# Performance work log

Hardware: AMD Instinct MI355X
Metric: run time of the kernel (lower is better)

Reference implementation:

```python
import jax, jax.numpy as jnp
import numpy as np

NUM_CHANNELS = 64
EMBED_DIM = 64
NUM_HEADS = 8


def _hilbert_filter(T):
    # scipy.signal.hilbert frequency-domain multiplier
    h = np.zeros(T, dtype=np.float32)
    if T % 2 == 0:
        h[0] = 1.0
        h[T // 2] = 1.0
        h[1:T // 2] = 2.0
    else:
        h[0] = 1.0
        h[1:(T + 1) // 2] = 2.0
    return jnp.asarray(h)


def setup_inputs() -> dict:
    key = jax.random.key(0)
    ks = jax.random.split(key, 12)
    B, C, T, E = 32, NUM_CHANNELS, 8192, EMBED_DIM
    inp = {
        "x": jax.random.normal(ks[0], (B, C, T), dtype=jnp.float32),
        "electrode_embeddings": jax.random.normal(ks[1], (C, E), dtype=jnp.float32),
        "w1": jax.random.normal(ks[2], (E, 2 * E), dtype=jnp.float32),
        "b1": jnp.zeros((2 * E,), dtype=jnp.float32),
        "w2": jax.random.normal(ks[3], (2 * E, E), dtype=jnp.float32),
        "b2": jnp.zeros((E,), dtype=jnp.float32),
        "in_proj_w": jax.random.normal(ks[4], (3 * E, E), dtype=jnp.float32) * (1.0 / np.sqrt(E)),
        "in_proj_b": jnp.zeros((3 * E,), dtype=jnp.float32),
        "out_proj_w": jax.random.normal(ks[5], (E, E), dtype=jnp.float32) * (1.0 / np.sqrt(E)),
        "out_proj_b": jnp.zeros((E,), dtype=jnp.float32),
    }
    return inp


def _connectivity(x):
    # x: (B, C, T) real. PLV_{ij} = |mean_t exp(i (phi_i - phi_j))|
    B, C, T = x.shape
    h = _hilbert_filter(T)
    analytic = jnp.fft.ifft(jnp.fft.fft(x, axis=-1) * h, axis=-1)  # complex64
    Z = analytic / jnp.abs(analytic)  # unit-magnitude phasors exp(i*phi)
    plv = jnp.abs(jnp.einsum("bit,bjt->bij", Z, jnp.conj(Z))) / T
    # original never fills the diagonal -> zero it
    eye = jnp.eye(C, dtype=plv.dtype)
    return plv * (1.0 - eye)


def _mha(h, in_proj_w, in_proj_b, out_proj_w, out_proj_b):
    # torch nn.MultiheadAttention, batch_first, self-attention
    B, N, E = h.shape
    H, D = NUM_HEADS, E // NUM_HEADS
    qkv = h @ in_proj_w.T + in_proj_b  # (B, N, 3E)
    q, k, v = jnp.split(qkv, 3, axis=-1)

    def heads(t):
        return t.reshape(B, N, H, D).transpose(0, 2, 1, 3)  # (B, H, N, D)

    q, k, v = heads(q), heads(k), heads(v)
    scores = jnp.einsum("bhqd,bhkd->bhqk", q, k) / jnp.sqrt(jnp.asarray(D, h.dtype))
    attn = jax.nn.softmax(scores, axis=-1)
    out = jnp.einsum("bhqk,bhkd->bhqd", attn, v)
    out = out.transpose(0, 2, 1, 3).reshape(B, N, E)
    return out @ out_proj_w.T + out_proj_b


def reference(x, electrode_embeddings, w1, b1, w2, b2,
              in_proj_w, in_proj_b, out_proj_w, out_proj_b):
    B = x.shape[0]
    connectivity = _connectivity(x)  # (B, C, C)
    node_features = jnp.broadcast_to(electrode_embeddings[None], (B,) + electrode_embeddings.shape)
    # GCN layer 1
    h1 = jnp.einsum("bij,bjf->bif", connectivity, node_features @ w1) + b1
    h1 = jax.nn.relu(h1)
    # GCN layer 2
    h2 = jnp.einsum("bij,bjf->bif", connectivity, h1 @ w2) + b2
    graph_features = _mha(h2, in_proj_w, in_proj_b, out_proj_w, out_proj_b)
    return connectivity, graph_features, h2
```

## Files before the change

kernel.cpp:

```cpp
#include <hip/hip_runtime.h>
#include <math.h>

#define T_LEN 8192
#define NS_G 8

typedef float  f32x4 __attribute__((ext_vector_type(4)));
typedef _Float16 f16x8 __attribute__((ext_vector_type(8)));
typedef float  cpx   __attribute__((ext_vector_type(2)));
typedef _Float16 f16h2 __attribute__((ext_vector_type(2)));

#define CADD(d, a, b) \
    asm("v_pk_add_f32 %0, %1, %2" : "=v"(d) : "v"(a), "v"(b))
#define CSUB(d, a, b) \
    asm("v_pk_add_f32 %0, %1, %2 neg_lo:[0,1] neg_hi:[0,1]" : "=v"(d) : "v"(a), "v"(b))
#define CFMA(d, s, a, b) \
    asm("v_pk_fma_f32 %0, %1, %2, %3" : "=v"(d) : "v"(s), "v"(a), "v"(b))
#define CMUL(d, x, w) do { cpx _t_;                                            \
    asm("v_pk_mul_f32 %0, %1, %2 op_sel:[0,0] op_sel_hi:[1,0]"                 \
        : "=v"(_t_) : "v"(x), "v"(w));                                         \
    asm("v_pk_fma_f32 %0, %1, %2, %3 op_sel:[1,1,0] op_sel_hi:[0,1,1] "        \
        "neg_lo:[1,0,0] neg_hi:[0,0,0]"                                        \
        : "=v"(d) : "v"(x), "v"(w), "v"(_t_)); } while (0)

__device__ __forceinline__ constexpr int br5(int r) {
    return ((r & 1) << 4) | ((r & 2) << 2) | (r & 4) | ((r & 8) >> 2) | ((r & 16) >> 4);
}

__device__ __forceinline__ f16h2 pk16(cpx v) {
    return (f16h2)__builtin_amdgcn_cvt_pkrtz(v.x, v.y);
}
__device__ __forceinline__ cpx unpk16(f16h2 h) {
    cpx v; v.x = (float)h.x; v.y = (float)h.y; return v;
}

__device__ __forceinline__ void fft32p(cpx* v)
{
    constexpr float TR[16] = {
        1.0f, 0.9807852804f, 0.9238795325f, 0.8314696123f,
        0.7071067812f, 0.5555702330f, 0.3826834324f, 0.1950903220f,
        0.0f, -0.1950903220f, -0.3826834324f, -0.5555702330f,
        -0.7071067812f, -0.8314696123f, -0.9238795325f, -0.9807852804f };
    constexpr float TI[16] = {
        0.0f, -0.1950903220f, -0.3826834324f, -0.5555702330f,
        -0.7071067812f, -0.8314696123f, -0.9238795325f, -0.9807852804f,
        -1.0f, -0.9807852804f, -0.9238795325f, -0.8314696123f,
        -0.7071067812f, -0.5555702330f, -0.3826834324f, -0.1950903220f };
    #pragma unroll
    for (int s = 0; s < 5; ++s) {
        const int half = 16 >> s;
        #pragma unroll
        for (int g = 0; g < (1 << s); ++g) {
            #pragma unroll
            for (int jj = 0; jj < half; ++jj) {
                const int i1 = g * (half << 1) + jj;
                const int i2 = i1 + half;
                const int q = jj << s;
                cpx a = v[i1], b = v[i2], u, d;
                CADD(u, a, b);
                CSUB(d, a, b);
                v[i1] = u;
                if (q == 0) {
                    v[i2] = d;
                } else {
                    cpx w; w.x = TR[q]; w.y = TI[q];
                    cpx o; CMUL(o, d, w);
                    v[i2] = o;
                }
            }
        }
    }
}

__device__ __forceinline__ void big_fftp(cpx* v, f16h2* lds, int t, int j, int row)
{
    fft32p(v);
    const float base1 = -7.669903939428206e-4f * (float)t;
    #pragma unroll
    for (int r = 0; r < 32; ++r) {
        const int k1 = br5(r);
        if (k1) {
            float c, s; __sincosf(base1 * (float)k1, &s, &c);
            cpx w; w.x = c; w.y = s;
            cpx o; CMUL(o, v[r], w);
            v[r] = o;
        }
    }
    __syncthreads();
    #pragma unroll
    for (int r = 0; r < 32; ++r) {
        int a = (br5(r) << 8) + t;
        lds[a ^ (((a >> 8) & 7) << 3)] = pk16(v[r]);
    }
    __syncthreads();
    #pragma unroll
    for (int m1 = 0; m1 < 32; ++m1) {
        int a = (row << 8) + (m1 << 3) + j;
        v[m1] = unpk16(lds[a ^ (((a >> 8) & 7) << 3)]);
    }

    fft32p(v);
    const float base2 = -0.02454369260617026f * (float)j;
    #pragma unroll
    for (int r = 0; r < 32; ++r) {
        const int k1p = br5(r);
        if (k1p) {
            float c, s; __sincosf(base2 * (float)k1p, &s, &c);
            cpx w; w.x = c; w.y = s;
            cpx o; CMUL(o, v[r], w);
            v[r] = o;
        }
    }
    const float R2v = 0.7071067811865475f;
    const int jm = j & 3;
    cpx w1; w1.x = 1.f; w1.y = 0.f;
    if (j >= 4) {
        w1.x = (jm == 0) ? 1.f : (jm == 1) ? R2v : (jm == 2) ? 0.f : -R2v;
        w1.y = (jm == 0) ? 0.f : (jm == 1) ? -R2v : (jm == 2) ? -1.f : -R2v;
    }
    cpx sg1; sg1.x = sg1.y = (j < 4) ? 1.f : -1.f;
    cpx sg2; sg2.x = sg2.y = (j & 2) ? -1.f : 1.f;
    const bool tw2 = (j & 2) && (j & 1);
    cpx w2; w2.x = tw2 ? 0.f : 1.f; w2.y = tw2 ? -1.f : 0.f;
    cpx sg3; sg3.x = sg3.y = (j & 1) ? -1.f : 1.f;
    #pragma unroll
    for (int r = 0; r < 32; ++r) {
        cpx o, sres, tres;
        o.x = __shfl_xor(v[r].x, 4);
        o.y = __shfl_xor(v[r].y, 4);
        CFMA(sres, sg1, v[r], o);
        CMUL(tres, sres, w1);
        o.x = __shfl_xor(tres.x, 2);
        o.y = __shfl_xor(tres.y, 2);
        CFMA(sres, sg2, tres, o);
        CMUL(tres, sres, w2);
        o.x = __shfl_xor(tres.x, 1);
        o.y = __shfl_xor(tres.y, 1);
        CFMA(sres, sg3, tres, o);
        v[r] = sres;
    }
}

__global__ __launch_bounds__(256)
__attribute__((amdgpu_num_vgpr(168)))
void fft_hilbert_kernel(
    const float* __restrict__ x, _Float16* __restrict__ zr,
    _Float16* __restrict__ zi)
{
    __shared__ f16h2 lds[8192];
    const int sig = blockIdx.x;
    const int t = threadIdx.x;
    const int j = t & 7, row = t >> 3;
    const int br3j = ((j & 1) << 2) | (j & 2) | ((j & 4) >> 2);

    cpx v[32];
    const float* xp = x + (size_t)sig * T_LEN;
    #pragma unroll
    for (int n1 = 0; n1 < 32; ++n1) { v[n1].x = xp[(n1 << 8) + t]; v[n1].y = 0.f; }

    big_fftp(v, lds, t, j, row);

    #pragma unroll
    for (int r = 0; r < 32; ++r) {
        const int k = row + (br5(r) << 5) + (br3j << 10);
        const float h = (k == 0 || k == 4096) ? 1.f : (k < 4096 ? 2.f : 0.f);
        v[r].x = v[r].x * h;
        v[r].y = -v[r].y * h;
    }

    __syncthreads();
    #pragma unroll
    for (int r = 0; r < 32; ++r) {
        int a = row + (br5(r) << 5) + (br3j << 10);
        lds[a ^ (((a >> 10) & 7) << 3)] = pk16(v[r]);
    }
    __syncthreads();
    #pragma unroll
    for (int n1 = 0; n1 < 32; ++n1) {
        int a = (n1 << 8) + t;
        v[n1] = unpk16(lds[a ^ (((a >> 10) & 7) << 3)]);
    }

    big_fftp(v, lds, t, j, row);

    _Float16* zrp = zr + (size_t)sig * T_LEN;
    _Float16* zip = zi + (size_t)sig * T_LEN;
    #pragma unroll
    for (int r = 0; r < 32; ++r) {
        float ar = v[r].x, ai = -v[r].y;
        float inv = rsqrtf(ar * ar + ai * ai);
        zrp[(r << 8) + t] = (_Float16)(ar * inv);
        zip[(r << 8) + t] = (_Float16)(ai * inv);
    }
}

#define GS 72
__global__ __launch_bounds__(256) void gram_kernel(
    const _Float16* __restrict__ zr, const _Float16* __restrict__ zi,
    float* __restrict__ part)
{
    __shared__ _Float16 ReS[64 * GS];
    __shared__ _Float16 ImS[64 * GS];
    const int b = blockIdx.x, sl = blockIdx.y, tid = threadIdx.x;
    const int w = tid >> 6, lane = tid & 63;
    const int mrow = lane & 15, quad = lane >> 4;

    f32x4 acc_re[4], acc_i1[4], acc_i2[4];
    #pragma unroll
    for (int tn = 0; tn < 4; ++tn) {
        acc_re[tn] = (f32x4)0.f; acc_i1[tn] = (f32x4)0.f; acc_i2[tn] = (f32x4)0.f;
    }

    const int k0 = sl * (T_LEN / NS_G);
    const int r0 = tid >> 3, r1 = r0 + 32;
    const int c8 = (tid & 7) * 8;
    const size_t gb = (size_t)b * 64 * T_LEN + k0;

    uint4 pr0 = *(const uint4*)&zr[gb + (size_t)r0 * T_LEN + c8];
    uint4 pi0 = *(const uint4*)&zi[gb + (size_t)r0 * T_LEN + c8];
    uint4 pr1 = *(const uint4*)&zr[gb + (size_t)r1 * T_LEN + c8];
    uint4 pi1 = *(const uint4*)&zi[gb + (size_t)r1 * T_LEN + c8];

    const int NCH = (T_LEN / NS_G) / 64;
    for (int chunk = 0; chunk < NCH; ++chunk) {
        __syncthreads();
        *(uint4*)&ReS[r0 * GS + c8] = pr0;
        *(uint4*)&ImS[r0 * GS + c8] = pi0;
        *(uint4*)&ReS[r1 * GS + c8] = pr1;
        *(uint4*)&ImS[r1 * GS + c8] = pi1;
        __syncthreads();
        if (chunk + 1 < NCH) {
            const size_t gn = gb + (chunk + 1) * 64;
            pr0 = *(const uint4*)&zr[gn + (size_t)r0 * T_LEN + c8];
            pi0 = *(const uint4*)&zi[gn + (size_t)r0 * T_LEN + c8];
            pr1 = *(const uint4*)&zr[gn + (size_t)r1 * T_LEN + c8];
            pi1 = *(const uint4*)&zi[gn + (size_t)r1 * T_LEN + c8];
        }
        #pragma unroll
        for (int ks = 0; ks < 2; ++ks) {
            const int koff = ks * 32 + quad * 8;
            f16x8 a_re = *(f16x8*)&ReS[(w * 16 + mrow) * GS + koff];
            f16x8 a_im = *(f16x8*)&ImS[(w * 16 + mrow) * GS + koff];
            #pragma unroll
            for (int tn = 0; tn < 4; ++tn) {
                f16x8 b_re = *(f16x8*)&ReS[(tn * 16 + mrow) * GS + koff];
                f16x8 b_im = *(f16x8*)&ImS[(tn * 16 + mrow) * GS + koff];
                acc_re[tn] = __builtin_amdgcn_mfma_f32_16x16x32_f16(a_re, b_re, acc_re[tn], 0, 0, 0);
                acc_re[tn] = __builtin_amdgcn_mfma_f32_16x16x32_f16(a_im, b_im, acc_re[tn], 0, 0, 0);
                acc_i1[tn] = __builtin_amdgcn_mfma_f32_16x16x32_f16(a_im, b_re, acc_i1[tn], 0, 0, 0);
                acc_i2[tn] = __builtin_amdgcn_mfma_f32_16x16x32_f16(a_re, b_im, acc_i2[tn], 0, 0, 0);
            }
        }
    }

    float2* pp = (float2*)part + (size_t)(b * NS_G + sl) * 4096;
    #pragma unroll
    for (int tn = 0; tn < 4; ++tn)
        #pragma unroll
        for (int reg = 0; reg < 4; ++reg) {
            int m = w * 16 + quad * 4 + reg;
            int n = tn * 16 + mrow;
            float2 vv;
            vv.x = acc_re[tn][reg];
            vv.y = acc_i1[tn][reg] - acc_i2[tn][reg];
            pp[m * 64 + n] = vv;
        }
}

__global__ __launch_bounds__(1024) void gnn_mha_kernel(
    const float* __restrict__ part, const float* __restrict__ emb,
    const float* __restrict__ w1,   const float* __restrict__ b1,
    const float* __restrict__ w2,   const float* __restrict__ b2,
    const float* __restrict__ ipw,  const float* __restrict__ ipb,
    const float* __restrict__ opw,  const float* __restrict__ opb,
    float* __restrict__ out0, float* __restrict__ out1,
    float* __restrict__ out2)
{
    __shared__ float S[16384];
    const int b = blockIdx.x, tid = threadIdx.x;
    const int lane = tid & 63, w = tid >> 6;
    const int i0 = w * 4;

    const float2* pf = (const float2*)part;
    for (int e = tid; e < 4096; e += 1024) {
        float gr = 0.f, gi = 0.f;
        #pragma unroll
        for (int s = 0; s < NS_G; ++s) {
            float2 vv = pf[(size_t)(b * NS_G + s) * 4096 + e];
            gr += vv.x; gi += vv.y;
        }
        int i = e >> 6, jj = e & 63;
        float val = (i == jj) ? 0.f
                              : sqrtf(gr * gr + gi * gi) * (1.0f / 8192.0f);
        S[e] = val;
        out0[(size_t)b * 4096 + e] = val;
    }
    __syncthreads();

    {
        float acc[4] = {0.f, 0.f, 0.f, 0.f};
        #pragma unroll 8
        for (int k = 0; k < 64; ++k) {
            float ev = emb[k * 64 + lane];
            #pragma unroll
            for (int r = 0; r < 4; ++r)
                acc[r] = fmaf(S[(i0 + r) * 64 + k], ev, acc[r]);
        }
        #pragma unroll
        for (int r = 0; r < 4; ++r) S[4096 + (i0 + r) * 64 + lane] = acc[r];
    }
    __syncthreads();

    {
        float a0[4] = {0.f, 0.f, 0.f, 0.f}, a1[4] = {0.f, 0.f, 0.f, 0.f};
        #pragma unroll 8
        for (int k = 0; k < 64; ++k) {
            float wa = w1[k * 128 + lane];
            float wb = w1[k * 128 + 64 + lane];
            #pragma unroll
            for (int r = 0; r < 4; ++r) {
                float m = S[4096 + (i0 + r) * 64 + k];
                a0[r] = fmaf(m, wa, a0[r]);
                a1[r] = fmaf(m, wb, a1[r]);
            }
        }
        float bb0 = b1[lane], bb1 = b1[64 + lane];
        #pragma unroll
        for (int r = 0; r < 4; ++r) {
            S[8192 + (i0 + r) * 128 + lane]      = fmaxf(a0[r] + bb0, 0.f);
            S[8192 + (i0 + r) * 128 + 64 + lane] = fmaxf(a1[r] + bb1, 0.f);
        }
    }
    __syncthreads();

    {
        float acc[4] = {0.f, 0.f, 0.f, 0.f};
        #pragma unroll 8
        for (int c = 0; c < 128; ++c) {
            float wv = w2[c * 64 + lane];
            #pragma unroll
            for (int r = 0; r < 4; ++r)
                acc[r] = fmaf(S[8192 + (i0 + r) * 128 + c], wv, acc[r]);
        }
        __syncthreads();
        #pragma unroll
        for (int r = 0; r < 4; ++r) S[4096 + (i0 + r) * 64 + lane] = acc[r];
    }
    __syncthreads();

    {
        float acc[4] = {0.f, 0.f, 0.f, 0.f};
        #pragma unroll 8
        for (int k = 0; k < 64; ++k) {
            float pv = S[4096 + k * 64 + lane];
            #pragma unroll
            for (int r = 0; r < 4; ++r)
                acc[r] = fmaf(S[(i0 + r) * 64 + k], pv, acc[r]);
        }
        float bb = b2[lane];
        #pragma unroll
        for (int r = 0; r < 4; ++r) {
            float vv = acc[r] + bb;
            S[(i0 + r) * 64 + lane] = vv;
            out2[(size_t)b * 4096 + (i0 + r) * 64 + lane] = vv;
        }
    }
    __syncthreads();

    {
        float aq[4] = {0.f, 0.f, 0.f, 0.f};
        float ak[4] = {0.f, 0.f, 0.f, 0.f};
        float av[4] = {0.f, 0.f, 0.f, 0.f};
        #pragma unroll 8
        for (int k = 0; k < 64; ++k) {
            float wq = ipw[lane * 64 + k];
            float wk = ipw[(64 + lane) * 64 + k];
            float wv = ipw[(128 + lane) * 64 + k];
            #pragma unroll
            for (int r = 0; r < 4; ++r) {
                float hv = S[(i0 + r) * 64 + k];
                aq[r] = fmaf(hv, wq, aq[r]);
                ak[r] = fmaf(hv, wk, ak[r]);
                av[r] = fmaf(hv, wv, av[r]);
            }
        }
        float bq = ipb[lane], bk = ipb[64 + lane], bv = ipb[128 + lane];
        __syncthreads();
        #pragma unroll
        for (int r = 0; r < 4; ++r) {
            S[4096  + (i0 + r) * 64 + lane] = aq[r] + bq;
            S[8192  + (i0 + r) * 64 + lane] = ak[r] + bk;
            S[12288 + (i0 + r) * 64 + lane] = av[r] + bv;
        }
    }
    __syncthreads();

    const int h = w >> 1;
    float kk[8];
    #pragma unroll
    for (int d = 0; d < 8; ++d) kk[d] = S[8192 + lane * 64 + h * 8 + d];
    __syncthreads();

    {
        const float iscale = 0.35355339059327373f;
        const int mc = lane >> 3, dd = lane & 7;
        for (int rr = 0; rr < 32; ++rr) {
            const int n = (w & 1) * 32 + rr;
            float s = 0.f;
            #pragma unroll
            for (int d = 0; d < 8; ++d)
                s = fmaf(S[4096 + n * 64 + h * 8 + d], kk[d], s);
            s *= iscale;
            float mx = s;
            #pragma unroll
            for (int off = 1; off < 64; off <<= 1)
                mx = fmaxf(mx, __shfl_xor(mx, off));
            float ev = __expf(s - mx);
            float sum = ev;
            #pragma unroll
            for (int off = 1; off < 64; off <<= 1)
                sum += __shfl_xor(sum, off);
            S[8192 + w * 68 + lane] = ev / sum;
            float o = 0.f;
            #pragma unroll
            for (int jx = 0; jx < 8; ++jx)
                o = fmaf(S[8192 + w * 68 + mc * 8 + jx],
                         S[12288 + (mc * 8 + jx) * 64 + h * 8 + dd], o);
            o += __shfl_xor(o, 8);
            o += __shfl_xor(o, 16);
            o += __shfl_xor(o, 32);
            if (lane < 8) S[n * 64 + h * 8 + lane] = o;
        }
    }
    __syncthreads();

    for (int e = tid; e < 4096; e += 1024) {
        int r = e >> 6, c = e & 63;
        S[8192 + r * 65 + c] = opw[e];
    }
    __syncthreads();

    {
        float acc[4] = {0.f, 0.f, 0.f, 0.f};
        #pragma unroll 8
        for (int c = 0; c < 64; ++c) {
            float wv = S[8192 + lane * 65 + c];
            #pragma unroll
            for (int r = 0; r < 4; ++r)
                acc[r] = fmaf(S[(i0 + r) * 64 + c], wv, acc[r]);
        }
        float ob = opb[lane];
        #pragma unroll
        for (int r = 0; r < 4; ++r)
            out1[(size_t)b * 4096 + (i0 + r) * 64 + lane] = acc[r] + ob;
    }
}

extern "C" void kernel_launch(void* const* d_in, const int* in_sizes, int n_in,
                              void* d_out, int out_size, void* d_ws, size_t ws_size,
                              hipStream_t stream)
{
    const float* x   = (const float*)d_in[0];
    const float* emb = (const float*)d_in[1];
    const float* w1  = (const float*)d_in[2];
    const float* b1  = (const float*)d_in[3];
    const float* w2  = (const float*)d_in[4];
    const float* b2  = (const float*)d_in[5];
    const float* ipw = (const float*)d_in[6];
    const float* ipb = (const float*)d_in[7];
    const float* opw = (const float*)d_in[8];
    const float* opb = (const float*)d_in[9];

    float* out  = (float*)d_out;
    float* out0 = out;
    float* out1 = out + 131072;
    float* out2 = out + 262144;

    _Float16* zr = (_Float16*)d_ws;
    _Float16* zi = zr + (size_t)2048 * T_LEN;
    float* part  = (float*)(zi + (size_t)2048 * T_LEN);

    hipLaunchKernelGGL(fft_hilbert_kernel, dim3(32 * 64), dim3(256), 0, stream,
                       x, zr, zi);
    hipLaunchKernelGGL(gram_kernel, dim3(32, NS_G), dim3(256), 0, stream,
                       zr, zi, part);
    hipLaunchKernelGGL(gnn_mha_kernel, dim3(32), dim3(1024), 0, stream,
                       part, emb, w1, b1, w2, b2, ipw, ipb, opw, opb,
                       out0, out1, out2);
}
```

Before: 333.4 us.

## Split Gram over more time slices, widen chunks, move PLV reduction to separate kernel

Doubles the number of time slices in the Gram kernel to launch more blocks, and widens each LDS chunk to 128 time samples so each chunk runs more MFMA steps per barrier. The partial-sum reduction and PLV computation move out of the single-block-per-batch GNN kernel into a new 128-block kernel, and the GNN kernel reads connectivity from the output buffer. The FFT kernel's VGPR cap is also lowered slightly. In exchange there is an extra kernel launch, twice the partial-sum traffic, and higher LDS and register use per Gram block.

After: 374.3 us. 1.12x slower.

```diff
diff --git a/kernel.cpp b/kernel.cpp
--- a/kernel.cpp
+++ b/kernel.cpp
@@ -2,7 +2,8 @@
 #include <math.h>
 
 #define T_LEN 8192
-#define NS_G 8
+#define NS_G 16
+#define GS2 136
 
 typedef float  f32x4 __attribute__((ext_vector_type(4)));
 typedef _Float16 f16x8 __attribute__((ext_vector_type(8)));
@@ -141,7 +142,7 @@
 }
 
 __global__ __launch_bounds__(256)
-__attribute__((amdgpu_num_vgpr(168)))
+__attribute__((amdgpu_num_vgpr(160)))
 void fft_hilbert_kernel(
     const float* __restrict__ x, _Float16* __restrict__ zr,
     _Float16* __restrict__ zi)
@@ -193,13 +194,12 @@
     }
 }
 
-#define GS 72
 __global__ __launch_bounds__(256) void gram_kernel(
     const _Float16* __restrict__ zr, const _Float16* __restrict__ zi,
     float* __restrict__ part)
 {
-    __shared__ _Float16 ReS[64 * GS];
-    __shared__ _Float16 ImS[64 * GS];
+    __shared__ _Float16 ReS[64 * GS2];
+    __shared__ _Float16 ImS[64 * GS2];
     const int b = blockIdx.x, sl = blockIdx.y, tid = threadIdx.x;
     const int w = tid >> 6, lane = tid & 63;
     const int mrow = lane & 15, quad = lane >> 4;
@@ -211,39 +211,43 @@
     }
 
     const int k0 = sl * (T_LEN / NS_G);
-    const int r0 = tid >> 3, r1 = r0 + 32;
-    const int c8 = (tid & 7) * 8;
+    const int rb = tid >> 4;
+    const int c8 = (tid & 15) * 8;
     const size_t gb = (size_t)b * 64 * T_LEN + k0;
 
-    uint4 pr0 = *(const uint4*)&zr[gb + (size_t)r0 * T_LEN + c8];
-    uint4 pi0 = *(const uint4*)&zi[gb + (size_t)r0 * T_LEN + c8];
-    uint4 pr1 = *(const uint4*)&zr[gb + (size_t)r1 * T_LEN + c8];
-    uint4 pi1 = *(const uint4*)&zi[gb + (size_t)r1 * T_LEN + c8];
-
-    const int NCH = (T_LEN / NS_G) / 64;
+    uint4 pr[4], pi[4];
+    #pragma unroll
+    for (int p = 0; p < 4; ++p) {
+        pr[p] = *(const uint4*)&zr[gb + (size_t)(rb + p * 16) * T_LEN + c8];
+        pi[p] = *(const uint4*)&zi[gb + (size_t)(rb + p * 16) * T_LEN + c8];
+    }
+
+    const int NCH = (T_LEN / NS_G) / 128;
     for (int chunk = 0; chunk < NCH; ++chunk) {
         __syncthreads();
-        *(uint4*)&ReS[r0 * GS + c8] = pr0;
-        *(uint4*)&ImS[r0 * GS + c8] = pi0;
-        *(uint4*)&ReS[r1 * GS + c8] = pr1;
-        *(uint4*)&ImS[r1 * GS + c8] = pi1;
+        #pragma unroll
+        for (int p = 0; p < 4; ++p) {
+            *(uint4*)&ReS[(rb + p * 16) * GS2 + c8] = pr[p];
+            *(uint4*)&ImS[(rb + p * 16) * GS2 + c8] = pi[p];
+        }
         __syncthreads();
         if (chunk + 1 < NCH) {
-            const size_t gn = gb + (chunk + 1) * 64;
-            pr0 = *(const uint4*)&zr[gn + (size_t)r0 * T_LEN + c8];
-            pi0 = *(const uint4*)&zi[gn + (size_t)r0 * T_LEN + c8];
-            pr1 = *(const uint4*)&zr[gn + (size_t)r1 * T_LEN + c8];
-            pi1 = *(const uint4*)&zi[gn + (size_t)r1 * T_LEN + c8];
-        }
-        #pragma unroll
-        for (int ks = 0; ks < 2; ++ks) {
+            const size_t gn = gb + (chunk + 1) * 128;
+            #pragma unroll
+            for (int p = 0; p < 4; ++p) {
+                pr[p] = *(const uint4*)&zr[gn + (size_t)(rb + p * 16) * T_LEN + c8];
+                pi[p] = *(const uint4*)&zi[gn + (size_t)(rb + p * 16) * T_LEN + c8];
+            }
+        }
+        #pragma unroll
+        for (int ks = 0; ks < 4; ++ks) {
             const int koff = ks * 32 + quad * 8;
-            f16x8 a_re = *(f16x8*)&ReS[(w * 16 + mrow) * GS + koff];
-            f16x8 a_im = *(f16x8*)&ImS[(w * 16 + mrow) * GS + koff];
+            f16x8 a_re = *(f16x8*)&ReS[(w * 16 + mrow) * GS2 + koff];
+            f16x8 a_im = *(f16x8*)&ImS[(w * 16 + mrow) * GS2 + koff];
             #pragma unroll
             for (int tn = 0; tn < 4; ++tn) {
-                f16x8 b_re = *(f16x8*)&ReS[(tn * 16 + mrow) * GS + koff];
-                f16x8 b_im = *(f16x8*)&ImS[(tn * 16 + mrow) * GS + koff];
+                f16x8 b_re = *(f16x8*)&ReS[(tn * 16 + mrow) * GS2 + koff];
+                f16x8 b_im = *(f16x8*)&ImS[(tn * 16 + mrow) * GS2 + koff];
                 acc_re[tn] = __builtin_amdgcn_mfma_f32_16x16x32_f16(a_re, b_re, acc_re[tn], 0, 0, 0);
                 acc_re[tn] = __builtin_amdgcn_mfma_f32_16x16x32_f16(a_im, b_im, acc_re[tn], 0, 0, 0);
                 acc_i1[tn] = __builtin_amdgcn_mfma_f32_16x16x32_f16(a_im, b_re, acc_i1[tn], 0, 0, 0);
@@ -266,34 +270,40 @@
         }
 }
 
+__global__ __launch_bounds__(256) void plv_kernel(
+    const float* __restrict__ part, float* __restrict__ out0)
+{
+    const int b = blockIdx.x, tid = threadIdx.x;
+    const float2* pf = (const float2*)part;
+    for (int e0 = tid; e0 < 1024; e0 += 256) {
+        int e = blockIdx.y * 1024 + e0;
+        float gr = 0.f, gi = 0.f;
+        #pragma unroll
+        for (int s = 0; s < NS_G; ++s) {
+            float2 v = pf[(size_t)(b * NS_G + s) * 4096 + e];
+            gr += v.x; gi += v.y;
+        }
+        int i = e >> 6, jj = e & 63;
+        float val = (i == jj) ? 0.f
+                              : sqrtf(gr * gr + gi * gi) * (1.0f / 8192.0f);
+        out0[(size_t)b * 4096 + e] = val;
+    }
+}
+
 __global__ __launch_bounds__(1024) void gnn_mha_kernel(
-    const float* __restrict__ part, const float* __restrict__ emb,
+    const float* __restrict__ conn, const float* __restrict__ emb,
     const float* __restrict__ w1,   const float* __restrict__ b1,
     const float* __restrict__ w2,   const float* __restrict__ b2,
     const float* __restrict__ ipw,  const float* __restrict__ ipb,
     const float* __restrict__ opw,  const float* __restrict__ opb,
-    float* __restrict__ out0, float* __restrict__ out1,
-    float* __restrict__ out2)
+    float* __restrict__ out1, float* __restrict__ out2)
 {
     __shared__ float S[16384];
     const int b = blockIdx.x, tid = threadIdx.x;
     const int lane = tid & 63, w = tid >> 6;
     const int i0 = w * 4;
 
-    const float2* pf = (const float2*)part;
-    for (int e = tid; e < 4096; e += 1024) {
-        float gr = 0.f, gi = 0.f;
-        #pragma unroll
-        for (int s = 0; s < NS_G; ++s) {
-            float2 vv = pf[(size_t)(b * NS_G + s) * 4096 + e];
-            gr += vv.x; gi += vv.y;
-        }
-        int i = e >> 6, jj = e & 63;
-        float val = (i == jj) ? 0.f
-                              : sqrtf(gr * gr + gi * gi) * (1.0f / 8192.0f);
-        S[e] = val;
-        out0[(size_t)b * 4096 + e] = val;
-    }
+    for (int e = tid; e < 4096; e += 1024) S[e] = conn[(size_t)b * 4096 + e];
     __syncthreads();
 
     {
@@ -483,7 +493,8 @@
                        x, zr, zi);
     hipLaunchKernelGGL(gram_kernel, dim3(32, NS_G), dim3(256), 0, stream,
                        zr, zi, part);
+    hipLaunchKernelGGL(plv_kernel, dim3(32, 4), dim3(256), 0, stream, part, out0);
     hipLaunchKernelGGL(gnn_mha_kernel, dim3(32), dim3(1024), 0, stream,
-                       part, emb, w1, b1, w2, b2, ipw, ipb, opw, opb,
-                       out0, out1, out2);
-}
+                       out0, emb, w1, b1, w2, b2, ipw, ipb, opw, opb,
+                       out1, out2);
+}
```
